# Performance work log

Measured on AMD Instinct MI355X. Metric: run time of the kernel, lower is better.

## Reference

```python
import jax, jax.numpy as jnp
import numpy as np

N_NODES = 100000
N_EDGES = 1600000
N_GRAPHS = 512
IN_CH = 128
FILT = 128
N_CONVS = 4  # 1 + n_rounds(3)


def setup_inputs() -> dict:
    key = jax.random.key(0)
    ks = jax.random.split(key, 10)
    x = jax.random.normal(ks[0], (N_NODES, IN_CH), dtype=jnp.float32)
    edge_index = jax.random.randint(ks[1], (2, N_EDGES), 0, N_NODES, dtype=jnp.int32)
    batch = jnp.sort(jax.random.randint(ks[2], (N_NODES,), 0, N_GRAPHS, dtype=jnp.int32))
    # GCNConv weights (in_channels == filter_size so all convs stack uniformly)
    s = 1.0 / np.sqrt(FILT)
    conv_w = jax.random.uniform(ks[3], (N_CONVS, IN_CH, FILT), jnp.float32, -s, s)
    conv_b = jnp.zeros((N_CONVS, FILT), jnp.float32)
    fc1_w = jax.random.uniform(ks[4], (FILT, FILT), jnp.float32, -s, s)
    fc1_b = jax.random.uniform(ks[5], (FILT,), jnp.float32, -s, s)
    fc2_w = jax.random.uniform(ks[6], (FILT, 1), jnp.float32, -s, s)
    fc2_b = jax.random.uniform(ks[7], (1,), jnp.float32, -s, s)
    return {"x": x, "edge_index": edge_index, "batch": batch, "batch_size": N_GRAPHS,
            "conv_w": conv_w, "conv_b": conv_b,
            "fc1_w": fc1_w, "fc1_b": fc1_b, "fc2_w": fc2_w, "fc2_b": fc2_b}


def _gcn_layer(x, W, b, src, dst, dinv):
    # GCNConv with improved=True: A_hat = A + 2I, sym-normalized by D_hat^{-1/2}
    h = x @ W                                   # [N, F]
    enorm = dinv[src] * dinv[dst]               # [E]
    agg = jax.ops.segment_sum(h[src] * enorm[:, None], dst, num_segments=N_NODES)
    self_loop = (2.0 * dinv * dinv)[:, None] * h
    return agg + self_loop + b


def reference(x, edge_index, batch, batch_size, conv_w, conv_b, fc1_w, fc1_b, fc2_w, fc2_b):
    src, dst = edge_index[0], edge_index[1]
    # degree including improved self-loop weight 2
    deg = jax.ops.segment_sum(jnp.ones((N_EDGES,), x.dtype), dst, num_segments=N_NODES) + 2.0
    dinv = jax.lax.rsqrt(deg)
    for i in range(N_CONVS):
        x = _gcn_layer(x, conv_w[i], conv_b[i], src, dst, dinv)
        x = jax.nn.relu(x)
        # dropout is identity in eval mode
    # global mean pool over graphs
    sums = jax.ops.segment_sum(x, batch, num_segments=batch_size)
    cnt = jax.ops.segment_sum(jnp.ones((N_NODES,), x.dtype), batch, num_segments=batch_size)
    pooled = sums / jnp.maximum(cnt, 1.0)[:, None]   # [G, F]
    h = jax.nn.relu(pooled @ fc1_w + fc1_b)
    out = h @ fc2_w + fc2_b                          # [G, 1]
    return out[:, 0]
```

## Files before the change

kernel.cpp:

```cpp
#include <hip/hip_runtime.h>
#include <hip/hip_fp16.h>

#define N_NODES 100000
#define N_EDGES 1600000
#define N_GRAPHS 512
#define F 128
#define N_CONVS 4
#define SCAN_NBLK ((N_NODES + 1023) / 1024)
#define FILL_BLOCKS ((N_EDGES + 255) / 256)
#define NWIN 8
#define WIN_SZ ((N_NODES + NWIN - 1) / NWIN)

#define W2_STRIDE 132
#define W2_LAYER (128 * W2_STRIDE)

typedef __attribute__((ext_vector_type(8))) short short8;
typedef __attribute__((ext_vector_type(4))) float f32x4;

union FragU { uint4 u; short8 v; };
union HU4 { uint4 u; __half2 h[4]; };

__device__ __forceinline__ float4 fma4(float w, float4 v, float4 a) {
    a.x = fmaf(w, v.x, a.x); a.y = fmaf(w, v.y, a.y);
    a.z = fmaf(w, v.z, a.z); a.w = fmaf(w, v.w, a.w);
    return a;
}

__device__ __forceinline__ unsigned int pack_hilo(float f) {
    unsigned int u = __float_as_uint(f);
    unsigned int hb = u & 0xFFFF0000u;
    float d = f - __uint_as_float(hb);
    unsigned int lb = __float_as_uint(d) >> 16;
    return (u >> 16) | (lb << 16);
}


__global__ void count_kernel(const int* __restrict__ dst, int* __restrict__ cnt) {
    int e = blockIdx.x * blockDim.x + threadIdx.x;
    if (e < N_EDGES) atomicAdd(&cnt[dst[e]], 1);
}

__global__ void dinv_kernel(const int* __restrict__ cnt, float* __restrict__ dinv) {
    int n = blockIdx.x * blockDim.x + threadIdx.x;
    if (n < N_NODES) dinv[n] = rsqrtf((float)cnt[n] + 2.0f);
}

__global__ void scan1_kernel(const int* __restrict__ cnt, int* __restrict__ excl,
                             int* __restrict__ blksum) {
    __shared__ int sums[256];
    int t = threadIdx.x;
    int base = blockIdx.x * 1024 + t * 4;
    int v0 = 0, v1 = 0, v2 = 0, v3 = 0;
    if (base + 0 < N_NODES) v0 = cnt[base + 0];
    if (base + 1 < N_NODES) v1 = cnt[base + 1];
    if (base + 2 < N_NODES) v2 = cnt[base + 2];
    if (base + 3 < N_NODES) v3 = cnt[base + 3];
    int s = v0 + v1 + v2 + v3;
    sums[t] = s;
    __syncthreads();
    for (int off = 1; off < 256; off <<= 1) {
        int y = (t >= off) ? sums[t - off] : 0;
        __syncthreads();
        sums[t] += y;
        __syncthreads();
    }
    int pre = sums[t] - s;
    if (base + 0 < N_NODES) excl[base + 0] = pre;
    if (base + 1 < N_NODES) excl[base + 1] = pre + v0;
    if (base + 2 < N_NODES) excl[base + 2] = pre + v0 + v1;
    if (base + 3 < N_NODES) excl[base + 3] = pre + v0 + v1 + v2;
    if (t == 255) blksum[blockIdx.x] = sums[255];
}

__global__ void scan2_kernel(int* __restrict__ blksum, int nblk) {
    __shared__ int sh[128];
    int t = threadIdx.x;
    int v = (t < nblk) ? blksum[t] : 0;
    sh[t] = v;
    __syncthreads();
    for (int off = 1; off < 128; off <<= 1) {
        int y = (t >= off) ? sh[t - off] : 0;
        __syncthreads();
        sh[t] += y;
        __syncthreads();
    }
    if (t < nblk) blksum[t] = sh[t] - v;
}

__global__ void scan3_kernel(int* __restrict__ rowptr, const int* __restrict__ blksum,
                             int* __restrict__ fill) {
    int t = threadIdx.x;
    int base = blockIdx.x * 1024 + t * 4;
    int off = blksum[blockIdx.x];
#pragma unroll
    for (int i = 0; i < 4; i++) {
        int idx = base + i;
        if (idx < N_NODES) {
            int v = rowptr[idx] + off;
            rowptr[idx] = v;
            fill[idx] = v;
        }
    }
    if (blockIdx.x == 0 && t == 0) rowptr[N_NODES] = N_EDGES;
}


__global__ __launch_bounds__(256) void fillw_kernel(
        const int* __restrict__ src, const int* __restrict__ dst,
        const float* __restrict__ dinv, int* __restrict__ fill,
        int2* __restrict__ edges) {
    int b = blockIdx.x;
    int w = b & (NWIN - 1);
    int e = (b >> 3) * 256 + threadIdx.x;
    if (e < N_EDGES) {
        int d = dst[e];
        if (d / WIN_SZ == w) {
            int s = src[e];
            int pos = atomicAdd(&fill[d], 1);
            edges[pos] = make_int2(s, __float_as_int(dinv[s] * dinv[d]));
        }
    }
}


__global__ void wpack_kernel(const float* __restrict__ conv_w, unsigned int* __restrict__ W2g) {
    int idx = blockIdx.x * 256 + threadIdx.x;
    if (idx < N_CONVS * 16384) {
        int L = idx >> 14;
        int e = idx & 16383;
        int k = e >> 7;
        int n = e & 127;
        float f = conv_w[(size_t)L * 16384 + k * 128 + n];
        W2g[(size_t)L * W2_LAYER + n * W2_STRIDE + k] = pack_hilo(f);
    }
}


__global__ __launch_bounds__(256, 2) void gemm_mfma_kernel(const float* __restrict__ X,
                                                           const unsigned int* __restrict__ W2g,
                                                           __half* __restrict__ Hh) {
    __shared__ unsigned int wlds[128 * W2_STRIDE];
    int t = threadIdx.x;

    {
        const uint4* s4 = (const uint4*)W2g;
        uint4* d4 = (uint4*)wlds;
#pragma unroll
        for (int i = 0; i < 17; i++) {
            int idx = i * 256 + t;
            if (idx < (128 * W2_STRIDE) / 4) d4[idx] = s4[idx];
        }
    }
    __syncthreads();

    int w = t >> 6;
    int l = t & 63;
    int m = l & 15;
    int q = l >> 4;
    int r0 = blockIdx.x * 128 + w * 32 + m;
    int r1 = r0 + 16;
    int r0c = (r0 > N_NODES - 1) ? (N_NODES - 1) : r0;
    int r1c = (r1 > N_NODES - 1) ? (N_NODES - 1) : r1;
    const float4* X4 = (const float4*)X;

    uint4 a0[8], a1[8];
#pragma unroll
    for (int i = 0; i < 8; i++) {
        float4 xv = X4[(size_t)r0c * 32 + i * 4 + q];
        a0[i].x = pack_hilo(xv.x); a0[i].y = pack_hilo(xv.y);
        a0[i].z = pack_hilo(xv.z); a0[i].w = pack_hilo(xv.w);
        float4 yv = X4[(size_t)r1c * 32 + i * 4 + q];
        a1[i].x = pack_hilo(yv.x); a1[i].y = pack_hilo(yv.y);
        a1[i].z = pack_hilo(yv.z); a1[i].w = pack_hilo(yv.w);
    }

    f32x4 acc0[8], acc1[8];
#pragma unroll
    for (int nb = 0; nb < 8; nb++) {
        acc0[nb] = (f32x4){0.f, 0.f, 0.f, 0.f};
        acc1[nb] = (f32x4){0.f, 0.f, 0.f, 0.f};
    }

#pragma unroll
    for (int nb = 0; nb < 8; nb++) {
        const unsigned int* wb = &wlds[(nb * 16 + m) * W2_STRIDE];
#pragma unroll
        for (int i = 0; i < 8; i++) {
            uint4 b = *(const uint4*)(wb + i * 16 + q * 4);
            FragU fa0, fa1, fb, fr;
            fa0.u = a0[i]; fa1.u = a1[i]; fb.u = b;
            acc0[nb] = __builtin_amdgcn_mfma_f32_16x16x32_bf16(fa0.v, fb.v, acc0[nb], 0, 0, 0);
            acc1[nb] = __builtin_amdgcn_mfma_f32_16x16x32_bf16(fa1.v, fb.v, acc1[nb], 0, 0, 0);
            fr.u.x = (b.x >> 16) | (b.x << 16);
            fr.u.y = (b.y >> 16) | (b.y << 16);
            fr.u.z = (b.z >> 16) | (b.z << 16);
            fr.u.w = (b.w >> 16) | (b.w << 16);
            acc0[nb] = __builtin_amdgcn_mfma_f32_16x16x32_bf16(fa0.v, fr.v, acc0[nb], 0, 0, 0);
            acc1[nb] = __builtin_amdgcn_mfma_f32_16x16x32_bf16(fa1.v, fr.v, acc1[nb], 0, 0, 0);
        }
    }

    int rbase = blockIdx.x * 128 + w * 32 + q * 4;
#pragma unroll
    for (int nb = 0; nb < 8; nb++) {
#pragma unroll
        for (int r = 0; r < 4; r++) {
            int row = rbase + r;
            if (row < N_NODES) Hh[(size_t)row * F + nb * 16 + m] = __float2half(acc0[nb][r]);
            int row1 = row + 16;
            if (row1 < N_NODES) Hh[(size_t)row1 * F + nb * 16 + m] = __float2half(acc1[nb][r]);
        }
    }
}


__global__ __launch_bounds__(256) void agg_kernel(const uint4* __restrict__ H16,
                                                  const int* __restrict__ rowptr,
                                                  const int2* __restrict__ edges,
                                                  const float* __restrict__ dinv,
                                                  const float4* __restrict__ bias4,
                                                  float4* __restrict__ Xo4) {
    int node = blockIdx.x * 4 + (threadIdx.x >> 6);
    if (node >= N_NODES) return;
    int lane = threadIdx.x & 63;
    int c16 = lane & 15;
    int slot = lane >> 4;

    int lo = rowptr[node];
    int hi = rowptr[node + 1];
    int him1 = hi - 1;

    float4 aL = make_float4(0.f, 0.f, 0.f, 0.f);
    float4 aH = make_float4(0.f, 0.f, 0.f, 0.f);

    for (int i = lo + slot; i < hi; i += 16) {
        int s[4]; float w[4]; uint4 v[4];
#pragma unroll
        for (int j = 0; j < 4; j++) {
            int ij = i + 4 * j;
            int cj = (ij < him1) ? ij : him1;
            int2 e = edges[cj];
            s[j] = e.x;
            w[j] = (ij < hi) ? __int_as_float(e.y) : 0.f;
        }
#pragma unroll
        for (int j = 0; j < 4; j++) v[j] = H16[(size_t)s[j] * 16 + c16];
#pragma unroll
        for (int j = 0; j < 4; j++) {
            HU4 x; x.u = v[j];
            float2 p0 = __half22float2(x.h[0]);
            float2 p1 = __half22float2(x.h[1]);
            float2 p2 = __half22float2(x.h[2]);
            float2 p3 = __half22float2(x.h[3]);
            aL.x = fmaf(w[j], p0.x, aL.x); aL.y = fmaf(w[j], p0.y, aL.y);
            aL.z = fmaf(w[j], p1.x, aL.z); aL.w = fmaf(w[j], p1.y, aL.w);
            aH.x = fmaf(w[j], p2.x, aH.x); aH.y = fmaf(w[j], p2.y, aH.y);
            aH.z = fmaf(w[j], p3.x, aH.z); aH.w = fmaf(w[j], p3.y, aH.w);
        }
    }

    aL.x += __shfl_down(aL.x, 32, 64); aL.y += __shfl_down(aL.y, 32, 64);
    aL.z += __shfl_down(aL.z, 32, 64); aL.w += __shfl_down(aL.w, 32, 64);
    aH.x += __shfl_down(aH.x, 32, 64); aH.y += __shfl_down(aH.y, 32, 64);
    aH.z += __shfl_down(aH.z, 32, 64); aH.w += __shfl_down(aH.w, 32, 64);
    aL.x += __shfl_down(aL.x, 16, 64); aL.y += __shfl_down(aL.y, 16, 64);
    aL.z += __shfl_down(aL.z, 16, 64); aL.w += __shfl_down(aL.w, 16, 64);
    aH.x += __shfl_down(aH.x, 16, 64); aH.y += __shfl_down(aH.y, 16, 64);
    aH.z += __shfl_down(aH.z, 16, 64); aH.w += __shfl_down(aH.w, 16, 64);

    if (slot == 0) {
        float dn = dinv[node];
        float sw = 2.0f * dn * dn;
        HU4 x; x.u = H16[(size_t)node * 16 + c16];
        float2 p0 = __half22float2(x.h[0]);
        float2 p1 = __half22float2(x.h[1]);
        float2 p2 = __half22float2(x.h[2]);
        float2 p3 = __half22float2(x.h[3]);
        float4 bL = bias4[c16 * 2];
        float4 bH = bias4[c16 * 2 + 1];
        float4 rL, rH;
        rL.x = fmaxf(fmaf(sw, p0.x, aL.x) + bL.x, 0.f);
        rL.y = fmaxf(fmaf(sw, p0.y, aL.y) + bL.y, 0.f);
        rL.z = fmaxf(fmaf(sw, p1.x, aL.z) + bL.z, 0.f);
        rL.w = fmaxf(fmaf(sw, p1.y, aL.w) + bL.w, 0.f);
        rH.x = fmaxf(fmaf(sw, p2.x, aH.x) + bH.x, 0.f);
        rH.y = fmaxf(fmaf(sw, p2.y, aH.y) + bH.y, 0.f);
        rH.z = fmaxf(fmaf(sw, p3.x, aH.z) + bH.z, 0.f);
        rH.w = fmaxf(fmaf(sw, p3.y, aH.w) + bH.w, 0.f);
        Xo4[(size_t)node * 32 + c16 * 2]     = rL;
        Xo4[(size_t)node * 32 + c16 * 2 + 1] = rH;
    }
}


__global__ __launch_bounds__(256) void pool_fc_kernel(const float* __restrict__ x,
                                                      const int* __restrict__ batch,
                                                      const float* __restrict__ fc1w,
                                                      const float* __restrict__ fc1b,
                                                      const float* __restrict__ fc2w,
                                                      const float* __restrict__ fc2b,
                                                      float* __restrict__ out) {
    __shared__ float part[2][F];
    __shared__ float pooled[F];
    __shared__ int bnd[2];
    __shared__ float red[2];
    int g = blockIdx.x, t = threadIdx.x;
    int c = t & 127, hlf = t >> 7;

    if (t < 2) {
        int target = g + t;
        int lo = 0, hi = N_NODES;
        while (lo < hi) {
            int m = (lo + hi) >> 1;
            if (batch[m] < target) lo = m + 1;
            else hi = m;
        }
        bnd[t] = lo;
    }
    __syncthreads();
    int lo = bnd[0], hi = bnd[1];

    float s = 0.f;
    int n = lo + hlf;
    for (; n + 6 < hi; n += 8) {
        float v0 = x[(size_t)n * F + c];
        float v1 = x[(size_t)(n + 2) * F + c];
        float v2 = x[(size_t)(n + 4) * F + c];
        float v3 = x[(size_t)(n + 6) * F + c];
        s += (v0 + v1) + (v2 + v3);
    }
    for (; n < hi; n += 2) s += x[(size_t)n * F + c];
    part[hlf][c] = s;
    __syncthreads();

    if (t < F) {
        float cntf = fmaxf((float)(hi - lo), 1.0f);
        pooled[c] = (part[0][c] + part[1][c]) / cntf;
    }
    __syncthreads();

    if (t < F) {
        float acc = fc1b[t];
#pragma unroll 4
        for (int k = 0; k < F; k++) acc = fmaf(pooled[k], fc1w[k * F + t], acc);
        acc = fmaxf(acc, 0.f);

        float p = acc * fc2w[t];
#pragma unroll
        for (int o = 32; o > 0; o >>= 1) p += __shfl_down(p, o, 64);
        if ((t & 63) == 0) red[t >> 6] = p;
    }
    __syncthreads();
    if (t == 0) out[g] = red[0] + red[1] + fc2b[0];
}


extern "C" void kernel_launch(void* const* d_in, const int* in_sizes, int n_in,
                              void* d_out, int out_size, void* d_ws, size_t ws_size,
                              hipStream_t stream) {
    const float* x_in   = (const float*)d_in[0];
    const int*   eidx   = (const int*)d_in[1];
    const int*   batch  = (const int*)d_in[2];
    const float* conv_w = (const float*)d_in[4];
    const float* conv_b = (const float*)d_in[5];
    const float* fc1w   = (const float*)d_in[6];
    const float* fc1b   = (const float*)d_in[7];
    const float* fc2w   = (const float*)d_in[8];
    const float* fc2b   = (const float*)d_in[9];
    float* out = (float*)d_out;

    const int* src = eidx;
    const int* dst = eidx + N_EDGES;

    char* ws = (char*)d_ws;
    size_t off = 0;
    auto alloc = [&](size_t bytes) -> char* {
        char* p = ws + off;
        off += (bytes + 255) & ~(size_t)255;
        return p;
    };
    float*  bufA  = (float*)alloc((size_t)N_NODES * F * 4);
    __half* bufH  = (__half*)alloc((size_t)N_NODES * F * 2);
    float*  dinv  = (float*)alloc((size_t)N_NODES * 4);
    int*    cnt   = (int*)alloc((size_t)N_NODES * 4);
    int*    rowp  = (int*)alloc((size_t)(N_NODES + 1) * 4);
    int*    fill  = (int*)alloc((size_t)N_NODES * 4);
    int2*   edges = (int2*)alloc((size_t)N_EDGES * 8);
    unsigned int* W2g = (unsigned int*)alloc((size_t)N_CONVS * W2_LAYER * 4);
    int*    blks  = (int*)alloc(128 * 4);
    (void)ws_size; (void)in_sizes; (void)n_in; (void)out_size;

    hipMemsetAsync(cnt, 0, (size_t)N_NODES * 4, stream);
    count_kernel<<<(N_EDGES + 255) / 256, 256, 0, stream>>>(dst, cnt);
    dinv_kernel<<<(N_NODES + 255) / 256, 256, 0, stream>>>(cnt, dinv);
    scan1_kernel<<<SCAN_NBLK, 256, 0, stream>>>(cnt, rowp, blks);
    scan2_kernel<<<1, 128, 0, stream>>>(blks, SCAN_NBLK);
    scan3_kernel<<<SCAN_NBLK, 256, 0, stream>>>(rowp, blks, fill);
    wpack_kernel<<<(N_CONVS * 16384 + 255) / 256, 256, 0, stream>>>(conv_w, W2g);

    fillw_kernel<<<FILL_BLOCKS * NWIN, 256, 0, stream>>>(src, dst, dinv, fill, edges);

    const float* cur = x_in;
    for (int L = 0; L < N_CONVS; L++) {
        gemm_mfma_kernel<<<(N_NODES + 127) / 128, 256, 0, stream>>>(
            cur, W2g + (size_t)L * W2_LAYER, bufH);
        agg_kernel<<<(N_NODES + 3) / 4, 256, 0, stream>>>(
            (const uint4*)bufH, rowp, edges, dinv,
            (const float4*)(conv_b + (size_t)L * F), (float4*)bufA);
        cur = bufA;
    }

    pool_fc_kernel<<<N_GRAPHS, 256, 0, stream>>>(bufA, batch, fc1w, fc1b, fc2w, fc2b, out);
}
```

Before: 634.9 us.

## Replace 8-pass windowed edge fill with two-pass binning via staging buffer

```diff
diff --git a/kernel.cpp b/kernel.cpp
--- a/kernel.cpp
+++ b/kernel.cpp
@@ -7,10 +7,14 @@
 #define F 128
 #define N_CONVS 4
 #define SCAN_NBLK ((N_NODES + 1023) / 1024)
-#define FILL_BLOCKS ((N_EDGES + 255) / 256)
 #define NWIN 8
 #define WIN_SZ ((N_NODES + NWIN - 1) / NWIN)
 
+#define CHUNK 1024
+#define BINA_BLOCKS ((N_EDGES + CHUNK - 1) / CHUNK)
+#define STG_CAP 210000
+#define PB_CHUNKS ((STG_CAP + 255) / 256)
+
 #define W2_STRIDE 132
 #define W2_LAYER (128 * W2_STRIDE)
 
@@ -19,12 +23,6 @@
 
 union FragU { uint4 u; short8 v; };
 union HU4 { uint4 u; __half2 h[4]; };
-
-__device__ __forceinline__ float4 fma4(float w, float4 v, float4 a) {
-    a.x = fmaf(w, v.x, a.x); a.y = fmaf(w, v.y, a.y);
-    a.z = fmaf(w, v.z, a.z); a.w = fmaf(w, v.w, a.w);
-    return a;
-}
 
 __device__ __forceinline__ unsigned int pack_hilo(float f) {
     unsigned int u = __float_as_uint(f);
@@ -105,20 +103,76 @@
 }
 
 
-__global__ __launch_bounds__(256) void fillw_kernel(
+__global__ __launch_bounds__(256) void binA_kernel(
         const int* __restrict__ src, const int* __restrict__ dst,
+        int* __restrict__ cursor, int2* __restrict__ staging) {
+    __shared__ int2 buf[CHUNK];
+    __shared__ int cnt[NWIN];
+    __shared__ int off[NWIN];
+    __shared__ int gbase[NWIN];
+    int t = threadIdx.x;
+    if (t < NWIN) cnt[t] = 0;
+    __syncthreads();
+
+    int base = blockIdx.x * CHUNK;
+    int n = N_EDGES - base;
+    if (n > CHUNK) n = CHUNK;
+
+    int myw[4], myr[4], mys[4], myd[4];
+#pragma unroll
+    for (int j = 0; j < 4; j++) {
+        int li = t + j * 256;
+        if (li < n) {
+            int e = base + li;
+            int d = dst[e];
+            int s = src[e];
+            int w = d / WIN_SZ;
+            myw[j] = w; mys[j] = s; myd[j] = d;
+            myr[j] = atomicAdd(&cnt[w], 1);
+        } else {
+            myw[j] = -1;
+        }
+    }
+    __syncthreads();
+
+    if (t == 0) {
+        int o = 0;
+#pragma unroll
+        for (int w = 0; w < NWIN; w++) { off[w] = o; o += cnt[w]; }
+    }
+    __syncthreads();
+
+#pragma unroll
+    for (int j = 0; j < 4; j++)
+        if (myw[j] >= 0) buf[off[myw[j]] + myr[j]] = make_int2(mys[j], myd[j]);
+    if (t < NWIN) gbase[t] = atomicAdd(&cursor[t], cnt[t]);
+    __syncthreads();
+
+    for (int w = 0; w < NWIN; w++) {
+        int c = cnt[w], o = off[w], gb = gbase[w];
+        for (int i = t; i < c; i += 256) {
+            int idx = gb + i;
+            if (idx < STG_CAP)
+                staging[(size_t)w * STG_CAP + idx] = buf[o + i];
+        }
+    }
+}
+
+__global__ __launch_bounds__(256) void binB_kernel(
+        const int2* __restrict__ staging, const int* __restrict__ cursor,
         const float* __restrict__ dinv, int* __restrict__ fill,
         int2* __restrict__ edges) {
     int b = blockIdx.x;
     int w = b & (NWIN - 1);
-    int e = (b >> 3) * 256 + threadIdx.x;
-    if (e < N_EDGES) {
-        int d = dst[e];
-        if (d / WIN_SZ == w) {
-            int s = src[e];
-            int pos = atomicAdd(&fill[d], 1);
-            edges[pos] = make_int2(s, __float_as_int(dinv[s] * dinv[d]));
-        }
+    int count = cursor[w];
+    if (count > STG_CAP) count = STG_CAP;
+    int i = (b >> 3) * 256 + threadIdx.x;
+    if (i < count) {
+        int2 e = staging[(size_t)w * STG_CAP + i];
+        int s = e.x, d = e.y;
+        float wt = dinv[s] * dinv[d];
+        int pos = atomicAdd(&fill[d], 1);
+        edges[pos] = make_int2(s, __float_as_int(wt));
     }
 }
 
@@ -388,9 +442,12 @@
     int2*   edges = (int2*)alloc((size_t)N_EDGES * 8);
     unsigned int* W2g = (unsigned int*)alloc((size_t)N_CONVS * W2_LAYER * 4);
     int*    blks  = (int*)alloc(128 * 4);
+    int*    cursor = (int*)alloc(NWIN * 4);
+    int2*   staging = (int2*)bufA;
     (void)ws_size; (void)in_sizes; (void)n_in; (void)out_size;
 
     hipMemsetAsync(cnt, 0, (size_t)N_NODES * 4, stream);
+    hipMemsetAsync(cursor, 0, NWIN * 4, stream);
     count_kernel<<<(N_EDGES + 255) / 256, 256, 0, stream>>>(dst, cnt);
     dinv_kernel<<<(N_NODES + 255) / 256, 256, 0, stream>>>(cnt, dinv);
     scan1_kernel<<<SCAN_NBLK, 256, 0, stream>>>(cnt, rowp, blks);
@@ -398,7 +455,8 @@
     scan3_kernel<<<SCAN_NBLK, 256, 0, stream>>>(rowp, blks, fill);
     wpack_kernel<<<(N_CONVS * 16384 + 255) / 256, 256, 0, stream>>>(conv_w, W2g);
 
-    fillw_kernel<<<FILL_BLOCKS * NWIN, 256, 0, stream>>>(src, dst, dinv, fill, edges);
+    binA_kernel<<<BINA_BLOCKS, 256, 0, stream>>>(src, dst, cursor, staging);
+    binB_kernel<<<PB_CHUNKS * NWIN, 256, 0, stream>>>(staging, cursor, dinv, fill, edges);
 
     const float* cur = x_in;
     for (int L = 0; L < N_CONVS; L++) {
```

Measured after the change: 662.4 us. 1.04x slower.

## Replace windowed atomic CSR fill with two-pass shared-memory binning sort

Applied to the files above, without the earlier changes.

```diff
diff --git a/kernel.cpp b/kernel.cpp
--- a/kernel.cpp
+++ b/kernel.cpp
@@ -7,9 +7,13 @@
 #define F 128
 #define N_CONVS 4
 #define SCAN_NBLK ((N_NODES + 1023) / 1024)
-#define FILL_BLOCKS ((N_EDGES + 255) / 256)
-#define NWIN 8
-#define WIN_SZ ((N_NODES + NWIN - 1) / NWIN)
+
+#define SUBW 256
+#define SUBW_NODES 391
+#define SCAP 7040
+#define ACHUNK 4096
+#define BINA_BLOCKS ((N_EDGES + ACHUNK - 1) / ACHUNK)
+#define EBUF 8192
 
 #define W2_STRIDE 132
 #define W2_LAYER (128 * W2_STRIDE)
@@ -19,12 +23,6 @@
 
 union FragU { uint4 u; short8 v; };
 union HU4 { uint4 u; __half2 h[4]; };
-
-__device__ __forceinline__ float4 fma4(float w, float4 v, float4 a) {
-    a.x = fmaf(w, v.x, a.x); a.y = fmaf(w, v.y, a.y);
-    a.z = fmaf(w, v.z, a.z); a.w = fmaf(w, v.w, a.w);
-    return a;
-}
 
 __device__ __forceinline__ unsigned int pack_hilo(float f) {
     unsigned int u = __float_as_uint(f);
@@ -87,39 +85,101 @@
     if (t < nblk) blksum[t] = sh[t] - v;
 }
 
-__global__ void scan3_kernel(int* __restrict__ rowptr, const int* __restrict__ blksum,
-                             int* __restrict__ fill) {
+__global__ void scan3_kernel(int* __restrict__ rowptr, const int* __restrict__ blksum) {
     int t = threadIdx.x;
     int base = blockIdx.x * 1024 + t * 4;
     int off = blksum[blockIdx.x];
 #pragma unroll
     for (int i = 0; i < 4; i++) {
         int idx = base + i;
-        if (idx < N_NODES) {
-            int v = rowptr[idx] + off;
-            rowptr[idx] = v;
-            fill[idx] = v;
-        }
+        if (idx < N_NODES) rowptr[idx] += off;
     }
     if (blockIdx.x == 0 && t == 0) rowptr[N_NODES] = N_EDGES;
 }
 
 
-__global__ __launch_bounds__(256) void fillw_kernel(
+__global__ __launch_bounds__(256) void binA_kernel(
         const int* __restrict__ src, const int* __restrict__ dst,
-        const float* __restrict__ dinv, int* __restrict__ fill,
+        int* __restrict__ cursor, int2* __restrict__ staging) {
+    __shared__ int2 buf[ACHUNK];
+    __shared__ int cnt_s[SUBW], off_s[SUBW], cur_s[SUBW], gb_s[SUBW], sh[SUBW];
+    int t = threadIdx.x;
+    cnt_s[t] = 0;
+    __syncthreads();
+
+    int base = blockIdx.x * ACHUNK;
+    int n = N_EDGES - base;
+    if (n > ACHUNK) n = ACHUNK;
+
+    for (int li = t; li < n; li += 256)
+        atomicAdd(&cnt_s[dst[base + li] / SUBW_NODES], 1);
+    __syncthreads();
+
+    int v = cnt_s[t];
+    sh[t] = v;
+    __syncthreads();
+    for (int off = 1; off < SUBW; off <<= 1) {
+        int y = (t >= off) ? sh[t - off] : 0;
+        __syncthreads();
+        sh[t] += y;
+        __syncthreads();
+    }
+    int excl = sh[t] - v;
+    off_s[t] = excl;
+    cur_s[t] = excl;
+    gb_s[t] = atomicAdd(&cursor[t], v);
+    __syncthreads();
+
+    for (int li = t; li < n; li += 256) {
+        int e = base + li;
+        int d = dst[e], s = src[e];
+        int p = atomicAdd(&cur_s[d / SUBW_NODES], 1);
+        buf[p] = make_int2(s, d);
+    }
+    __syncthreads();
+
+    for (int i = t; i < n; i += 256) {
+        int2 e = buf[i];
+        int w = e.y / SUBW_NODES;
+        int idx = gb_s[w] + (i - off_s[w]);
+        if (idx < SCAP) staging[(size_t)w * SCAP + idx] = e;
+    }
+}
+
+__global__ __launch_bounds__(512) void binB_kernel(
+        const int2* __restrict__ staging, const int* __restrict__ cursor,
+        const int* __restrict__ rowptr, const float* __restrict__ dinv,
         int2* __restrict__ edges) {
-    int b = blockIdx.x;
-    int w = b & (NWIN - 1);
-    int e = (b >> 3) * 256 + threadIdx.x;
-    if (e < N_EDGES) {
-        int d = dst[e];
-        if (d / WIN_SZ == w) {
-            int s = src[e];
-            int pos = atomicAdd(&fill[d], 1);
-            edges[pos] = make_int2(s, __float_as_int(dinv[s] * dinv[d]));
-        }
-    }
+    __shared__ int rowl[SUBW_NODES + 1];
+    __shared__ int lcur[SUBW_NODES];
+    __shared__ int2 ebuf[EBUF];
+    int b = blockIdx.x, t = threadIdx.x;
+    int n0 = b * SUBW_NODES;
+    int n1 = n0 + SUBW_NODES;
+    if (n1 > N_NODES) n1 = N_NODES;
+    int nn = n1 - n0;
+
+    for (int i = t; i <= nn; i += 512) rowl[i] = rowptr[n0 + i];
+    for (int i = t; i < nn; i += 512) lcur[i] = 0;
+    __syncthreads();
+
+    int gb = rowl[0];
+    int total = rowl[nn] - gb;
+    int m = cursor[b];
+    if (m > SCAP) m = SCAP;
+
+    for (int i = t; i < m; i += 512) {
+        int2 e = staging[(size_t)b * SCAP + i];
+        int s = e.x, d = e.y;
+        float wt = dinv[s] * dinv[d];
+        int dl = d - n0;
+        int lpos = (rowl[dl] - gb) + atomicAdd(&lcur[dl], 1);
+        if (lpos < EBUF) ebuf[lpos] = make_int2(s, __float_as_int(wt));
+    }
+    __syncthreads();
+
+    for (int i = t; i < total; i += 512)
+        if (i < EBUF) edges[gb + i] = ebuf[i];
 }
 
 
@@ -384,21 +444,24 @@
     float*  dinv  = (float*)alloc((size_t)N_NODES * 4);
     int*    cnt   = (int*)alloc((size_t)N_NODES * 4);
     int*    rowp  = (int*)alloc((size_t)(N_NODES + 1) * 4);
-    int*    fill  = (int*)alloc((size_t)N_NODES * 4);
     int2*   edges = (int2*)alloc((size_t)N_EDGES * 8);
     unsigned int* W2g = (unsigned int*)alloc((size_t)N_CONVS * W2_LAYER * 4);
     int*    blks  = (int*)alloc(128 * 4);
+    int*    cursor = (int*)alloc(SUBW * 4);
+    int2*   staging = (int2*)bufA;
     (void)ws_size; (void)in_sizes; (void)n_in; (void)out_size;
 
     hipMemsetAsync(cnt, 0, (size_t)N_NODES * 4, stream);
+    hipMemsetAsync(cursor, 0, SUBW * 4, stream);
     count_kernel<<<(N_EDGES + 255) / 256, 256, 0, stream>>>(dst, cnt);
     dinv_kernel<<<(N_NODES + 255) / 256, 256, 0, stream>>>(cnt, dinv);
     scan1_kernel<<<SCAN_NBLK, 256, 0, stream>>>(cnt, rowp, blks);
     scan2_kernel<<<1, 128, 0, stream>>>(blks, SCAN_NBLK);
-    scan3_kernel<<<SCAN_NBLK, 256, 0, stream>>>(rowp, blks, fill);
+    scan3_kernel<<<SCAN_NBLK, 256, 0, stream>>>(rowp, blks);
     wpack_kernel<<<(N_CONVS * 16384 + 255) / 256, 256, 0, stream>>>(conv_w, W2g);
 
-    fillw_kernel<<<FILL_BLOCKS * NWIN, 256, 0, stream>>>(src, dst, dinv, fill, edges);
+    binA_kernel<<<BINA_BLOCKS, 256, 0, stream>>>(src, dst, cursor, staging);
+    binB_kernel<<<SUBW, 512, 0, stream>>>(staging, cursor, rowp, dinv, edges);
 
     const float* cur = x_in;
     for (int L = 0; L < N_CONVS; L++) {
```

After: 601.9 us. 1.05x faster.
